# Kernel tuning notes

Hardware: AMD Instinct MI355X
Metric: run time of the kernel (lower is better)

The kernel has to match this reference:

```python
import jax, jax.numpy as jnp
import numpy as np

B, S, D, A = 16, 2048, 512, 512

def setup_inputs() -> dict:
    key = jax.random.key(0)
    ks = jax.random.split(key, 7)
    scale = 1.0 / np.sqrt(D)
    return {
        "query": jax.random.normal(ks[0], (B, S, D), dtype=jnp.float32),
        "key_": jax.random.normal(ks[1], (B, S, D), dtype=jnp.float32),
        "value": jax.random.normal(ks[2], (B, S, D), dtype=jnp.float32),
        "Wq": jax.random.normal(ks[3], (D, A), dtype=jnp.float32) * scale,
        "Wk": jax.random.normal(ks[4], (D, A), dtype=jnp.float32) * scale,
        "Wv": jax.random.normal(ks[5], (D, A), dtype=jnp.float32) * scale,
        "Ws": jax.random.normal(ks[6], (A, 1), dtype=jnp.float32) * (1.0 / np.sqrt(A)),
    }

def reference(query, key_, value, Wq, Wk, Wv, Ws):
    # Dense projections (no bias): [B,S,D] @ [D,A] -> [B,S,A]
    q = jnp.einsum("bsd,da->bsa", query, Wq)
    k = jnp.einsum("bsd,da->bsa", key_, Wk)
    v = jnp.einsum("bsd,da->bsa", value, Wv)
    # Additive (Bahdanau) scores: tanh(q+k) @ Ws -> [B,S]
    scores = jnp.einsum("bsa,a->bs", jnp.tanh(q + k), Ws[:, 0])
    attention_weights = jax.nn.softmax(scores, axis=1)[..., None]  # [B,S,1]
    context_vector = jnp.sum(attention_weights * v, axis=1)        # [B,A]
    return context_vector, attention_weights
```

## Files before the change

### kernel.cpp

```cpp
#include <hip/hip_runtime.h>
#include <hip/hip_bf16.h>
#include <stdint.h>

#define B_ 16
#define S_ 2048
#define D_ 512
#define A_ 512

typedef __attribute__((ext_vector_type(4))) float f32x4;
typedef __attribute__((ext_vector_type(8))) short bf16x8;

__device__ inline unsigned short f2bf(float f) {
  union { float f; unsigned int u; } c; c.f = f;
  unsigned int u = c.u;
  unsigned int r = (u + 0x7fffu + ((u >> 16) & 1u)) >> 16;
  return (unsigned short)r;
}

__device__ inline unsigned pk2bf(float x, float y) {
  __hip_bfloat162 p = __float22bfloat162_rn(float2{x, y});
  union { __hip_bfloat162 h; unsigned u; } c; c.h = p;
  return c.u;
}

__device__ inline float fast_tanh(float x) {
  float e = __expf(2.0f * x);
  return 1.0f - 2.0f * __builtin_amdgcn_rcpf(e + 1.0f);
}

__device__ inline void gload_lds16(const void* g, void* l) {
  __builtin_amdgcn_global_load_lds((const __attribute__((address_space(1))) void*)g,
                                   (__attribute__((address_space(3))) void*)l, 16, 0, 0);
}

__global__ __launch_bounds__(256) void k0_pack_w(const float* __restrict__ Wq,
                                                 const float* __restrict__ Wk,
                                                 unsigned short* __restrict__ WT) {
  __shared__ unsigned short tile[64][65];
  int bid = blockIdx.x;
  int dt = bid & 15, at = bid >> 4;
  int d0 = dt * 64, a0 = at * 64;
  int t = threadIdx.x;
  int col = t & 63, rbase = t >> 6;
#pragma unroll
  for (int r8 = 0; r8 < 16; ++r8) {
    int row = r8 * 4 + rbase;
    int dcat = d0 + row;
    float f = (dcat < 512) ? Wq[(size_t)dcat * 512 + a0 + col]
                           : Wk[(size_t)(dcat - 512) * 512 + a0 + col];
    tile[row][col] = f2bf(f);
  }
  __syncthreads();
#pragma unroll
  for (int r8 = 0; r8 < 16; ++r8) {
    int arow = r8 * 4 + rbase;
    WT[(size_t)(a0 + arow) * 1024 + d0 + col] = tile[col][arow];
  }
}

__global__ __launch_bounds__(512, 2) void k1_scores(
    const float* __restrict__ Q, const float* __restrict__ K,
    const unsigned short* __restrict__ WT, const float* __restrict__ Wsv,
    float* __restrict__ score) {
  __shared__ unsigned short Al[2][128 * 32];
  __shared__ unsigned short Bl[2][512 * 32];

  const int t = threadIdx.x;
  const int lane = t & 63, w = t >> 6;
  const int frow = lane & 15, fsl = lane >> 4;
  const int row0 = (int)blockIdx.x * 128;

  const int ar = t >> 2, ak = (t & 3) * 8;
  const int abyte = ar * 64 + (((t & 3) ^ ((ar >> 1) & 3)) * 16);

  float4 rA0[2], rA1[2];

  auto issueA = [&](int p, float4* r) {
    const float* src = (p < 16) ? Q : K;
    const float* ap = src + (size_t)(row0 + ar) * 512 + ((p * 32) & 511) + ak;
    r[0] = *(const float4*)(ap);
    r[1] = *(const float4*)(ap + 4);
  };
  auto writeA = [&](const float4* r, int buf) {
    uint4 d;
    d.x = pk2bf(r[0].x, r[0].y);
    d.y = pk2bf(r[0].z, r[0].w);
    d.z = pk2bf(r[1].x, r[1].y);
    d.w = pk2bf(r[1].z, r[1].w);
    *(uint4*)((char*)&Al[buf][0] + abyte) = d;
  };
  auto stageB = [&](int p, int buf) {
#pragma unroll
    for (int q = 0; q < 4; ++q) {
      int pc = (w * 4 + q) * 64 + lane;
      int row = pc >> 2;
      int sl = (pc & 3) ^ ((row >> 1) & 3);
      const char* g = (const char*)WT + (size_t)row * 2048 + p * 64 + sl * 16;
      gload_lds16(g, (char*)&Bl[buf][0] + (size_t)(w * 4 + q) * 1024);
    }
  };

  f32x4 acc[8][4];
#pragma unroll
  for (int m = 0; m < 8; ++m)
#pragma unroll
    for (int n = 0; n < 4; ++n) acc[m][n] = (f32x4){0.f, 0.f, 0.f, 0.f};

  const int ch = (fsl ^ ((frow >> 1) & 3)) * 16;

  auto doMfma = [&](int CUR) {
    bf16x8 af[8], bfr[4];
#pragma unroll
    for (int m = 0; m < 8; ++m)
      af[m] = *(const bf16x8*)((const char*)&Al[CUR][0] + (m * 16 + frow) * 64 + ch);
#pragma unroll
    for (int n = 0; n < 4; ++n)
      bfr[n] = *(const bf16x8*)((const char*)&Bl[CUR][0] + (w * 64 + n * 16 + frow) * 64 + ch);
    __builtin_amdgcn_s_setprio(1);
#pragma unroll
    for (int m = 0; m < 8; ++m)
#pragma unroll
      for (int n = 0; n < 4; ++n)
        acc[m][n] = __builtin_amdgcn_mfma_f32_16x16x32_bf16(af[m], bfr[n], acc[m][n], 0, 0, 0);
    __builtin_amdgcn_s_setprio(0);
  };

  issueA(0, rA0);
  stageB(0, 0);
  __builtin_amdgcn_sched_barrier(0);
  issueA(1, rA1);
  writeA(rA0, 0);
  asm volatile("s_waitcnt vmcnt(2) lgkmcnt(0)" ::: "memory");
  __builtin_amdgcn_s_barrier();

  auto phase = [&](int p, int CUR, float4* rCur, const float4* rNext) {
    stageB(p + 1, CUR ^ 1);
    __builtin_amdgcn_sched_barrier(0);
    issueA(p + 2, rCur);
    doMfma(CUR);
    writeA(rNext, CUR ^ 1);
    asm volatile("s_waitcnt vmcnt(2) lgkmcnt(0)" ::: "memory");
    __builtin_amdgcn_s_barrier();
  };

  for (int kt2 = 0; kt2 < 15; ++kt2) {
    phase(2 * kt2 + 0, 0, rA0, rA1);
    phase(2 * kt2 + 1, 1, rA1, rA0);
  }

  stageB(31, 1);
  doMfma(0);
  writeA(rA1, 1);
  asm volatile("s_waitcnt vmcnt(0) lgkmcnt(0)" ::: "memory");
  __builtin_amdgcn_s_barrier();
  doMfma(1);

  float wsv[4];
#pragma unroll
  for (int n = 0; n < 4; ++n) wsv[n] = Wsv[w * 64 + n * 16 + frow];
  __syncthreads();
  float* scw = (float*)&Al[0][0];
#pragma unroll
  for (int m = 0; m < 8; ++m) {
#pragma unroll
    for (int ii = 0; ii < 4; ++ii) {
      float s = 0.f;
#pragma unroll
      for (int n = 0; n < 4; ++n)
        s += fast_tanh(acc[m][n][ii]) * wsv[n];
      s += __shfl_xor(s, 1);
      s += __shfl_xor(s, 2);
      s += __shfl_xor(s, 4);
      s += __shfl_xor(s, 8);
      if (frow == 0) scw[w * 128 + m * 16 + fsl * 4 + ii] = s;
    }
  }
  __syncthreads();
  if (t < 128) {
    float s = 0.f;
#pragma unroll
    for (int ww = 0; ww < 8; ++ww) s += scw[ww * 128 + t];
    score[row0 + t] = s;
  }
}

__global__ __launch_bounds__(256) void k3_vsum(const float* __restrict__ value,
                                               const float* __restrict__ score,
                                               float* __restrict__ upart,
                                               float* __restrict__ outw) {
  int bid = blockIdx.x;
  int dh = bid & 1, sc = (bid >> 1) & 15, b = bid >> 5;
  int t = threadIdx.x;
  int lane = t & 63, wave = t >> 6;
  int dg = t & 63, sg = t >> 6;
  __shared__ float red[4], red2[4];
  __shared__ float wl[128];
  __shared__ f32x4 redv[4][64];

  float v[8];
  float mx = -1e30f;
#pragma unroll
  for (int e = 0; e < 8; ++e) {
    float p = score[(size_t)b * S_ + e * 256 + t];
    v[e] = p;
    mx = fmaxf(mx, p);
  }
  for (int off = 1; off < 64; off <<= 1) mx = fmaxf(mx, __shfl_xor(mx, off));
  if (lane == 0) red[wave] = mx;
  __syncthreads();
  mx = fmaxf(fmaxf(red[0], red[1]), fmaxf(red[2], red[3]));
  float sum = 0.f;
#pragma unroll
  for (int e = 0; e < 8; ++e) sum += expf(v[e] - mx);
  for (int off = 1; off < 64; off <<= 1) sum += __shfl_xor(sum, off);
  if (lane == 0) red2[wave] = sum;
  __syncthreads();
  sum = red2[0] + red2[1] + red2[2] + red2[3];
  float inv = 1.f / sum;

  int s0 = sc * 128;
  if (t < 128) {
    float ww = expf(score[(size_t)b * S_ + s0 + t] - mx) * inv;
    wl[t] = ww;
    if (dh == 0) outw[(size_t)b * S_ + s0 + t] = ww;
  }
  __syncthreads();

  const float* vp = value + ((size_t)b * S_ + s0) * 512 + dh * 256 + dg * 4;
  f32x4 a = (f32x4){0.f, 0.f, 0.f, 0.f};
  for (int s = sg; s < 128; s += 4) {
    float4 v4 = *(const float4*)(vp + (size_t)s * 512);
    float ws = wl[s];
    a[0] += ws * v4.x; a[1] += ws * v4.y; a[2] += ws * v4.z; a[3] += ws * v4.w;
  }
  redv[sg][dg] = a;
  __syncthreads();
  if (sg == 0) {
    f32x4 r = redv[0][dg] + redv[1][dg] + redv[2][dg] + redv[3][dg];
    float* dst = upart + (size_t)(sc * 16 + b) * 512 + dh * 256 + dg * 4;
    dst[0] = r[0]; dst[1] = r[1]; dst[2] = r[2]; dst[3] = r[3];
  }
}

__global__ __launch_bounds__(512) void k4_ctx(const float* __restrict__ upart,
                                              const float* __restrict__ Wv,
                                              float* __restrict__ out) {
  int b = blockIdx.x, t = threadIdx.x;
  __shared__ float ul[512];
  float u = 0.f;
#pragma unroll
  for (int c = 0; c < 16; ++c) u += upart[(size_t)(c * 16 + b) * 512 + t];
  ul[t] = u;
  __syncthreads();
  float acc = 0.f;
#pragma unroll 8
  for (int d = 0; d < 512; ++d) acc += ul[d] * Wv[(size_t)d * 512 + t];
  out[(size_t)b * 512 + t] = acc;
}

extern "C" void kernel_launch(void* const* d_in, const int* in_sizes, int n_in,
                              void* d_out, int out_size, void* d_ws, size_t ws_size,
                              hipStream_t stream) {
  const float* Q  = (const float*)d_in[0];
  const float* Kk = (const float*)d_in[1];
  const float* V  = (const float*)d_in[2];
  const float* Wq = (const float*)d_in[3];
  const float* Wk = (const float*)d_in[4];
  const float* Wv = (const float*)d_in[5];
  const float* Ws = (const float*)d_in[6];
  float* out = (float*)d_out;

  char* ws = (char*)d_ws;
  unsigned short* WT = (unsigned short*)ws;
  float* score = (float*)(ws + (1 << 20));
  float* upart = (float*)(ws + (1 << 20) + (512 << 10));

  float* outw = out + B_ * A_;

  k0_pack_w<<<dim3(128), dim3(256), 0, stream>>>(Wq, Wk, WT);
  k1_scores<<<dim3(256), dim3(512), 0, stream>>>(Q, Kk, WT, Ws, score);
  k3_vsum<<<dim3(512), dim3(256), 0, stream>>>(V, score, upart, outw);
  k4_ctx<<<dim3(16), dim3(512), 0, stream>>>(upart, Wv, out);
}
```

Before: 96.29 us.

## Retile score GEMM into 256x256 tiles with split-column partial scores

The fused Q/K projection GEMM now uses 256-row by 256-column tiles with a K-step of 64 and a 2x4 wave grid. Each block produces partial scores for half the attention columns, and the softmax kernel sums the two halves. This raises arithmetic intensity per LDS load and halves the number of K iterations. The main loop is split into four sub-phases that interleave global loads and LDS writes with MFMAs. In exchange each Q/K row is read twice, once per column half, LDS usage grows to 128KB, and there is an extra partial-sum buffer. A swizzled block order is added so that column pairs share L2.

```diff
diff --git a/kernel.cpp b/kernel.cpp
--- a/kernel.cpp
+++ b/kernel.cpp
@@ -6,6 +6,7 @@
 #define S_ 2048
 #define D_ 512
 #define A_ 512
+#define M_TOT (B_ * S_)
 
 typedef __attribute__((ext_vector_type(4))) float f32x4;
 typedef __attribute__((ext_vector_type(8))) short bf16x8;
@@ -61,42 +62,51 @@
 __global__ __launch_bounds__(512, 2) void k1_scores(
     const float* __restrict__ Q, const float* __restrict__ K,
     const unsigned short* __restrict__ WT, const float* __restrict__ Wsv,
-    float* __restrict__ score) {
-  __shared__ unsigned short Al[2][128 * 32];
-  __shared__ unsigned short Bl[2][512 * 32];
+    float* __restrict__ partial) {
+  __shared__ unsigned short Ab[2][256 * 64];
+  __shared__ unsigned short Bb[2][256 * 64];
 
   const int t = threadIdx.x;
   const int lane = t & 63, w = t >> 6;
   const int frow = lane & 15, fsl = lane >> 4;
-  const int row0 = (int)blockIdx.x * 128;
-
-  const int ar = t >> 2, ak = (t & 3) * 8;
-  const int abyte = ar * 64 + (((t & 3) ^ ((ar >> 1) & 3)) * 16);
-
-  float4 rA0[2], rA1[2];
-
-  auto issueA = [&](int p, float4* r) {
-    const float* src = (p < 16) ? Q : K;
-    const float* ap = src + (size_t)(row0 + ar) * 512 + ((p * 32) & 511) + ak;
-    r[0] = *(const float4*)(ap);
+  const int wr = w >> 2, wc = w & 3;
+
+  const int bid = (int)blockIdx.x;
+  const int wg = (bid & 7) * 32 + (bid >> 3);
+  const int strip = wg >> 1, cb = wg & 1;
+  const int row0 = strip * 256, col0 = cb * 256;
+
+  const int ar = t >> 2, aq = t & 3;
+
+  float4 ra0[4], ra1[4];
+
+  auto issueA = [&](int kt, int h, float4* r) {
+    const float* src = (kt < 8) ? Q : K;
+    const float* ap = src + (size_t)(row0 + h * 128 + ar) * 512 + (kt & 7) * 64 + aq * 16;
+    r[0] = *(const float4*)(ap + 0);
     r[1] = *(const float4*)(ap + 4);
+    r[2] = *(const float4*)(ap + 8);
+    r[3] = *(const float4*)(ap + 12);
   };
-  auto writeA = [&](const float4* r, int buf) {
-    uint4 d;
-    d.x = pk2bf(r[0].x, r[0].y);
-    d.y = pk2bf(r[0].z, r[0].w);
-    d.z = pk2bf(r[1].x, r[1].y);
-    d.w = pk2bf(r[1].z, r[1].w);
-    *(uint4*)((char*)&Al[buf][0] + abyte) = d;
+  auto writeA = [&](int d, int h, const float4* r) {
+    uint4 d0, d1;
+    d0.x = pk2bf(r[0].x, r[0].y); d0.y = pk2bf(r[0].z, r[0].w);
+    d0.z = pk2bf(r[1].x, r[1].y); d0.w = pk2bf(r[1].z, r[1].w);
+    d1.x = pk2bf(r[2].x, r[2].y); d1.y = pk2bf(r[2].z, r[2].w);
+    d1.z = pk2bf(r[3].x, r[3].y); d1.w = pk2bf(r[3].z, r[3].w);
+    char* base = (char*)&Ab[d][0] + h * 16384 + ar * 128;
+    int c0 = (aq * 2) ^ (ar & 7), c1 = (aq * 2 + 1) ^ (ar & 7);
+    *(uint4*)(base + c0 * 16) = d0;
+    *(uint4*)(base + c1 * 16) = d1;
   };
-  auto stageB = [&](int p, int buf) {
-#pragma unroll
-    for (int q = 0; q < 4; ++q) {
-      int pc = (w * 4 + q) * 64 + lane;
-      int row = pc >> 2;
-      int sl = (pc & 3) ^ ((row >> 1) & 3);
-      const char* g = (const char*)WT + (size_t)row * 2048 + p * 64 + sl * 16;
-      gload_lds16(g, (char*)&Bl[buf][0] + (size_t)(w * 4 + q) * 1024);
+  auto stageB = [&](int d, int kt, int h) {
+#pragma unroll
+    for (int q = 0; q < 2; ++q) {
+      int p = q * 512 + t;
+      int brow = p >> 3, c = p & 7;
+      const char* g = (const char*)WT + (size_t)(col0 + h * 128 + brow) * 2048
+                      + kt * 128 + ((c ^ (brow & 7)) * 16);
+      gload_lds16(g, (char*)&Bb[d][0] + h * 16384 + (size_t)(q * 512 + w * 64) * 16);
     }
   };
 
@@ -106,86 +116,105 @@
 #pragma unroll
     for (int n = 0; n < 4; ++n) acc[m][n] = (f32x4){0.f, 0.f, 0.f, 0.f};
 
-  const int ch = (fsl ^ ((frow >> 1) & 3)) * 16;
-
-  auto doMfma = [&](int CUR) {
-    bf16x8 af[8], bfr[4];
-#pragma unroll
-    for (int m = 0; m < 8; ++m)
-      af[m] = *(const bf16x8*)((const char*)&Al[CUR][0] + (m * 16 + frow) * 64 + ch);
-#pragma unroll
-    for (int n = 0; n < 4; ++n)
-      bfr[n] = *(const bf16x8*)((const char*)&Bl[CUR][0] + (w * 64 + n * 16 + frow) * 64 + ch);
-    __builtin_amdgcn_s_setprio(1);
-#pragma unroll
-    for (int m = 0; m < 8; ++m)
-#pragma unroll
-      for (int n = 0; n < 4; ++n)
-        acc[m][n] = __builtin_amdgcn_mfma_f32_16x16x32_bf16(af[m], bfr[n], acc[m][n], 0, 0, 0);
-    __builtin_amdgcn_s_setprio(0);
-  };
-
-  issueA(0, rA0);
-  stageB(0, 0);
-  __builtin_amdgcn_sched_barrier(0);
-  issueA(1, rA1);
-  writeA(rA0, 0);
-  asm volatile("s_waitcnt vmcnt(2) lgkmcnt(0)" ::: "memory");
+#define PHASE(d, mh, nh, STAGE) do {                                           \
+    bf16x8 fa[2][4], fb[2][2];                                                 \
+    _Pragma("unroll") for (int ks = 0; ks < 2; ++ks) {                         \
+      _Pragma("unroll") for (int j = 0; j < 4; ++j) {                          \
+        int r = wr * 128 + (mh) * 64 + j * 16 + frow;                          \
+        fa[ks][j] = *(const bf16x8*)((const char*)&Ab[d][0] + r * 128          \
+                     + (((ks * 4 + fsl) ^ (r & 7)) * 16));                     \
+      }                                                                        \
+      _Pragma("unroll") for (int n2 = 0; n2 < 2; ++n2) {                       \
+        int r = wc * 64 + (nh) * 32 + n2 * 16 + frow;                          \
+        fb[ks][n2] = *(const bf16x8*)((const char*)&Bb[d][0] + r * 128         \
+                     + (((ks * 4 + fsl) ^ (r & 7)) * 16));                     \
+      }                                                                        \
+    }                                                                          \
+    STAGE;                                                                     \
+    __builtin_amdgcn_s_barrier();                                              \
+    asm volatile("s_waitcnt lgkmcnt(0)" ::: "memory");                         \
+    __builtin_amdgcn_sched_barrier(0);                                         \
+    __builtin_amdgcn_s_setprio(1);                                             \
+    _Pragma("unroll") for (int ks = 0; ks < 2; ++ks)                           \
+      _Pragma("unroll") for (int j = 0; j < 4; ++j)                            \
+        _Pragma("unroll") for (int n2 = 0; n2 < 2; ++n2)                       \
+          acc[(mh) * 4 + j][(nh) * 2 + n2] =                                   \
+            __builtin_amdgcn_mfma_f32_16x16x32_bf16(fa[ks][j], fb[ks][n2],     \
+                acc[(mh) * 4 + j][(nh) * 2 + n2], 0, 0, 0);                    \
+    __builtin_amdgcn_s_setprio(0);                                             \
+    __builtin_amdgcn_s_barrier();                                              \
+  } while (0)
+
+  issueA(0, 0, ra0);
+  issueA(0, 1, ra1);
+  stageB(0, 0, 0);
+  stageB(0, 0, 1);
+  writeA(0, 0, ra0);
+  writeA(0, 1, ra1);
+  issueA(1, 0, ra0);
+  issueA(1, 1, ra1);
+  asm volatile("s_waitcnt vmcnt(8) lgkmcnt(0)" ::: "memory");
   __builtin_amdgcn_s_barrier();
 
-  auto phase = [&](int p, int CUR, float4* rCur, const float4* rNext) {
-    stageB(p + 1, CUR ^ 1);
-    __builtin_amdgcn_sched_barrier(0);
-    issueA(p + 2, rCur);
-    doMfma(CUR);
-    writeA(rNext, CUR ^ 1);
-    asm volatile("s_waitcnt vmcnt(2) lgkmcnt(0)" ::: "memory");
-    __builtin_amdgcn_s_barrier();
-  };
-
-  for (int kt2 = 0; kt2 < 15; ++kt2) {
-    phase(2 * kt2 + 0, 0, rA0, rA1);
-    phase(2 * kt2 + 1, 1, rA1, rA0);
-  }
-
-  stageB(31, 1);
-  doMfma(0);
-  writeA(rA1, 1);
-  asm volatile("s_waitcnt vmcnt(0) lgkmcnt(0)" ::: "memory");
-  __builtin_amdgcn_s_barrier();
-  doMfma(1);
-
-  float wsv[4];
-#pragma unroll
-  for (int n = 0; n < 4; ++n) wsv[n] = Wsv[w * 64 + n * 16 + frow];
-  __syncthreads();
-  float* scw = (float*)&Al[0][0];
-#pragma unroll
-  for (int m = 0; m < 8; ++m) {
-#pragma unroll
-    for (int ii = 0; ii < 4; ++ii) {
-      float s = 0.f;
-#pragma unroll
-      for (int n = 0; n < 4; ++n)
-        s += fast_tanh(acc[m][n][ii]) * wsv[n];
-      s += __shfl_xor(s, 1);
-      s += __shfl_xor(s, 2);
-      s += __shfl_xor(s, 4);
-      s += __shfl_xor(s, 8);
-      if (frow == 0) scw[w * 128 + m * 16 + fsl * 4 + ii] = s;
+  for (int kt = 0; kt < 15; ++kt) {
+    const int d = kt & 1;
+    PHASE(d, 0, 0, { writeA(d ^ 1, 0, ra0); });
+    PHASE(d, 0, 1, { writeA(d ^ 1, 1, ra1); stageB(d ^ 1, kt + 1, 0); });
+    PHASE(d, 1, 0, { stageB(d ^ 1, kt + 1, 1); if (kt < 14) issueA(kt + 2, 0, ra0); });
+    PHASE(d, 1, 1, {
+      if (kt < 14) {
+        issueA(kt + 2, 1, ra1);
+        asm volatile("s_waitcnt vmcnt(8)" ::: "memory");
+      } else {
+        asm volatile("s_waitcnt vmcnt(0)" ::: "memory");
+      }
+    });
+  }
+  PHASE(1, 0, 0, {});
+  PHASE(1, 0, 1, {});
+  PHASE(1, 1, 0, {});
+  PHASE(1, 1, 1, {});
+#undef PHASE
+
+  float wsv2[2][2];
+#pragma unroll
+  for (int nh = 0; nh < 2; ++nh)
+#pragma unroll
+    for (int n2 = 0; n2 < 2; ++n2)
+      wsv2[nh][n2] = Wsv[col0 + wc * 64 + nh * 32 + n2 * 16 + frow];
+
+  float* scw = (float*)&Ab[0][0];
+  __syncthreads();
+#pragma unroll
+  for (int mh = 0; mh < 2; ++mh) {
+#pragma unroll
+    for (int j = 0; j < 4; ++j) {
+#pragma unroll
+      for (int ii = 0; ii < 4; ++ii) {
+        float s = 0.f;
+#pragma unroll
+        for (int nh = 0; nh < 2; ++nh)
+#pragma unroll
+          for (int n2 = 0; n2 < 2; ++n2)
+            s += fast_tanh(acc[mh * 4 + j][nh * 2 + n2][ii]) * wsv2[nh][n2];
+        s += __shfl_xor(s, 1);
+        s += __shfl_xor(s, 2);
+        s += __shfl_xor(s, 4);
+        s += __shfl_xor(s, 8);
+        if (frow == 0)
+          scw[wc * 256 + wr * 128 + mh * 64 + j * 16 + fsl * 4 + ii] = s;
+      }
     }
   }
   __syncthreads();
-  if (t < 128) {
-    float s = 0.f;
-#pragma unroll
-    for (int ww = 0; ww < 8; ++ww) s += scw[ww * 128 + t];
-    score[row0 + t] = s;
+  if (t < 256) {
+    float s = scw[t] + scw[256 + t] + scw[512 + t] + scw[768 + t];
+    partial[(size_t)cb * M_TOT + row0 + t] = s;
   }
 }
 
 __global__ __launch_bounds__(256) void k3_vsum(const float* __restrict__ value,
-                                               const float* __restrict__ score,
+                                               const float* __restrict__ partial,
                                                float* __restrict__ upart,
                                                float* __restrict__ outw) {
   int bid = blockIdx.x;
@@ -201,7 +230,8 @@
   float mx = -1e30f;
 #pragma unroll
   for (int e = 0; e < 8; ++e) {
-    float p = score[(size_t)b * S_ + e * 256 + t];
+    size_t o = (size_t)b * S_ + e * 256 + t;
+    float p = partial[o] + partial[M_TOT + o];
     v[e] = p;
     mx = fmaxf(mx, p);
   }
@@ -220,9 +250,10 @@
 
   int s0 = sc * 128;
   if (t < 128) {
-    float ww = expf(score[(size_t)b * S_ + s0 + t] - mx) * inv;
+    size_t o = (size_t)b * S_ + s0 + t;
+    float ww = expf(partial[o] + partial[M_TOT + o] - mx) * inv;
     wl[t] = ww;
-    if (dh == 0) outw[(size_t)b * S_ + s0 + t] = ww;
+    if (dh == 0) outw[o] = ww;
   }
   __syncthreads();
 
@@ -272,13 +303,13 @@
 
   char* ws = (char*)d_ws;
   unsigned short* WT = (unsigned short*)ws;
-  float* score = (float*)(ws + (1 << 20));
-  float* upart = (float*)(ws + (1 << 20) + (512 << 10));
+  float* partial = (float*)(ws + (1 << 20));
+  float* upart   = (float*)(ws + (1 << 20) + (512 << 10));
 
   float* outw = out + B_ * A_;
 
   k0_pack_w<<<dim3(128), dim3(256), 0, stream>>>(Wq, Wk, WT);
-  k1_scores<<<dim3(256), dim3(512), 0, stream>>>(Q, Kk, WT, Ws, score);
-  k3_vsum<<<dim3(512), dim3(256), 0, stream>>>(V, score, upart, outw);
+  k1_scores<<<dim3(256), dim3(512), 0, stream>>>(Q, Kk, WT, Ws, partial);
+  k3_vsum<<<dim3(512), dim3(256), 0, stream>>>(V, partial, upart, outw);
   k4_ctx<<<dim3(16), dim3(512), 0, stream>>>(upart, Wv, out);
 }
```

Result: slower. 109.2 us (+13.4%).
